# Kernel tuning notes

Measured on AMD Instinct MI355X. Metric: run time of the kernel, lower is better.

## Reference

```python
import jax, jax.numpy as jnp
import numpy as np

B, S, D, H = 4, 1024, 1024, 16
HD = D // H  # head_dim = 64


def setup_inputs() -> dict:
    key = jax.random.key(0)
    ks = jax.random.split(key, 12)
    inp = {
        "query": jax.random.normal(ks[0], (B, S, D), jnp.float32),
        "key": jax.random.normal(ks[1], (B, S, D), jnp.float32),
        "value": jax.random.normal(ks[2], (B, S, D), jnp.float32),
        # padding mask: 0 = masked, 1 = keep; broadcastable to [B,H,Sq,Sk]
        "mask": jax.random.randint(ks[3], (B, 1, 1, S), 0, 2, jnp.int32),
        # Dense params (Glorot-ish scale)
        "Wq": jax.random.normal(ks[4], (D, D), jnp.float32) / np.sqrt(D),
        "bq": jnp.zeros((D,), jnp.float32),
        "Wk": jax.random.normal(ks[5], (D, D), jnp.float32) / np.sqrt(D),
        "bk": jnp.zeros((D,), jnp.float32),
        "Wv": jax.random.normal(ks[6], (D, D), jnp.float32) / np.sqrt(D),
        "bv": jnp.zeros((D,), jnp.float32),
        "Wo": jax.random.normal(ks[7], (D, D), jnp.float32) / np.sqrt(D),
        "bo": jnp.zeros((D,), jnp.float32),
    }
    return inp


def _split_heads(x):
    # [B, S, D] -> [B, H, S, HD]
    b, s, _ = x.shape
    return x.reshape(b, s, H, HD).transpose(0, 2, 1, 3)


def reference(query, key, value, mask, Wq, bq, Wk, bk, Wv, bv, Wo, bo):
    q = _split_heads(query @ Wq + bq)   # [B,H,S,HD]
    k = _split_heads(key @ Wk + bk)
    v = _split_heads(value @ Wv + bv)

    scale = jnp.sqrt(jnp.asarray(HD, q.dtype))
    energy = jnp.einsum("bhqd,bhkd->bhqk", q, k) / scale  # [B,H,S,S]
    energy = jnp.where(mask == 0, jnp.asarray(-1e10, energy.dtype), energy)
    attention = jax.nn.softmax(energy, axis=-1)
    # dropout is identity at inference
    x = jnp.einsum("bhqk,bhkd->bhqd", attention, v)       # [B,H,S,HD]
    x = x.transpose(0, 2, 1, 3).reshape(query.shape[0], -1, H * HD)  # [B,S,D]
    outputs = x @ Wo + bo
    return outputs, attention
```

## Files before the change

kernel.cpp:

```cpp
#include <hip/hip_runtime.h>

typedef short short8  __attribute__((ext_vector_type(8)));
typedef short short4v __attribute__((ext_vector_type(4)));
typedef float float4v __attribute__((ext_vector_type(4)));
typedef int   int4v   __attribute__((ext_vector_type(4)));

__device__ __forceinline__ short f2bf(float f) {
    unsigned u = __builtin_bit_cast(unsigned, f);
    u += 0x7fff + ((u >> 16) & 1);
    return (short)(u >> 16);
}

__global__ __launch_bounds__(256) void transpose4(
    const float* __restrict__ W0, const float* __restrict__ W1,
    const float* __restrict__ W2, const float* __restrict__ W3,
    short* __restrict__ T0, short* __restrict__ T1,
    short* __restrict__ T2, short* __restrict__ T3)
{
    __shared__ short Tl[64 * 72];
    const int tid = threadIdx.x;
    const int mat = blockIdx.x >> 8;
    const int t   = blockIdx.x & 255;
    const int k0 = (t >> 4) * 64, n0 = (t & 15) * 64;
    const float* W = mat == 0 ? W0 : mat == 1 ? W1 : mat == 2 ? W2 : W3;
    short*       T = mat == 0 ? T0 : mat == 1 ? T1 : mat == 2 ? T2 : T3;
    #pragma unroll
    for (int i = 0; i < 4; i++) {
        int c = tid + i * 256;
        int row = c >> 4, c4 = (c & 15) * 4;
        float4v v = *(const float4v*)&W[(size_t)(k0 + row) * 1024 + n0 + c4];
        short4v s = {f2bf(v[0]), f2bf(v[1]), f2bf(v[2]), f2bf(v[3])};
        *(short4v*)&Tl[row * 72 + c4] = s;
    }
    __syncthreads();
    #pragma unroll
    for (int i = 0; i < 2; i++) {
        int c = tid + i * 256;
        int nrow = c >> 3, k8 = (c & 7) * 8;
        short8 v;
        #pragma unroll
        for (int e = 0; e < 8; e++) v[e] = Tl[(k8 + e) * 72 + nrow];
        *(short8*)&T[(size_t)(n0 + nrow) * 1024 + k0 + k8] = v;
    }
}

template<int CMODE, bool A_BF16>
__global__ __launch_bounds__(256) void gemm_bt64(
    const void* __restrict__ Av, const short* __restrict__ Bt,
    const float* __restrict__ bias, void* __restrict__ Cv,
    int M, int N, int K)
{
    __shared__ short As[64 * 72];
    __shared__ short Bs[64 * 72];
    const int tid = threadIdx.x;
    const int m0 = blockIdx.x * 64, n0 = blockIdx.y * 64;
    const int w = tid >> 6, lid = tid & 63, quad = lid >> 4, l15 = lid & 15;
    const int wrow = (w >> 1) * 32, wcol = (w & 1) * 32;

    float4v acc[2][2];
    #pragma unroll
    for (int i = 0; i < 2; i++)
        #pragma unroll
        for (int j = 0; j < 2; j++) acc[i][j] = (float4v){0.f, 0.f, 0.f, 0.f};

    for (int kb = 0; kb < K; kb += 64) {
        if constexpr (A_BF16) {
            const short* A = (const short*)Av;
            #pragma unroll
            for (int i = 0; i < 2; i++) {
                int c = tid + i * 256;
                int row = c >> 3, k8 = (c & 7) * 8;
                *(short8*)&As[row * 72 + k8] =
                    *(const short8*)&A[(size_t)(m0 + row) * K + kb + k8];
            }
        } else {
            const float* A = (const float*)Av;
            #pragma unroll
            for (int i = 0; i < 4; i++) {
                int c = tid + i * 256;
                int row = c >> 4, c4 = (c & 15) * 4;
                float4v v = *(const float4v*)&A[(size_t)(m0 + row) * K + kb + c4];
                short4v s = {f2bf(v[0]), f2bf(v[1]), f2bf(v[2]), f2bf(v[3])};
                *(short4v*)&As[row * 72 + c4] = s;
            }
        }
        #pragma unroll
        for (int i = 0; i < 2; i++) {
            int c = tid + i * 256;
            int row = c >> 3, k8 = (c & 7) * 8;
            *(short8*)&Bs[row * 72 + k8] =
                *(const short8*)&Bt[(size_t)(n0 + row) * K + kb + k8];
        }
        __syncthreads();
        short8 ar0[2], ar1[2], br0[2], br1[2];
        #pragma unroll
        for (int i = 0; i < 2; i++) {
            ar0[i] = *(short8*)&As[(wrow + i * 16 + l15) * 72 + quad * 8];
            ar1[i] = *(short8*)&As[(wrow + i * 16 + l15) * 72 + 32 + quad * 8];
        }
        #pragma unroll
        for (int j = 0; j < 2; j++) {
            br0[j] = *(short8*)&Bs[(wcol + j * 16 + l15) * 72 + quad * 8];
            br1[j] = *(short8*)&Bs[(wcol + j * 16 + l15) * 72 + 32 + quad * 8];
        }
        #pragma unroll
        for (int i = 0; i < 2; i++)
            #pragma unroll
            for (int j = 0; j < 2; j++) {
                acc[i][j] = __builtin_amdgcn_mfma_f32_16x16x32_bf16(
                    ar0[i], br0[j], acc[i][j], 0, 0, 0);
                acc[i][j] = __builtin_amdgcn_mfma_f32_16x16x32_bf16(
                    ar1[i], br1[j], acc[i][j], 0, 0, 0);
            }
        __syncthreads();
    }

    #pragma unroll
    for (int j = 0; j < 2; j++) {
        int n = n0 + wcol + j * 16 + l15;
        float bj = bias[n];
        #pragma unroll
        for (int i = 0; i < 2; i++) {
            if constexpr (CMODE == 2) {
                short* Vt = (short*)Cv;
                int b = m0 >> 10;
                int sbase = (m0 & 1023) + wrow + i * 16 + quad * 4;
                short4v sv;
                #pragma unroll
                for (int r = 0; r < 4; r++) sv[r] = f2bf(acc[i][j][r] + bj);
                *(short4v*)&Vt[(size_t)b * 1048576 + (size_t)n * 1024 + sbase] = sv;
            } else {
                #pragma unroll
                for (int r = 0; r < 4; r++) {
                    int m = m0 + wrow + i * 16 + quad * 4 + r;
                    if constexpr (CMODE == 1)
                        ((float*)Cv)[(size_t)m * N + n] = acc[i][j][r] + bj;
                    else
                        ((short*)Cv)[(size_t)m * N + n] = f2bf(acc[i][j][r] + bj);
                }
            }
        }
    }
}

__global__ __launch_bounds__(256) void attn_kernel(
    const short* __restrict__ Qp, const short* __restrict__ Kp,
    const short* __restrict__ Vt, const int* __restrict__ mask,
    float* __restrict__ attnOut, short* __restrict__ X)
{
    __shared__ short KVl[128 * 72];
    __shared__ short Pl[16 * 136];
    __shared__ int   maskl[1024];
    __shared__ float redmx[4][16];
    __shared__ float redsm[4][16];

    const int tid = threadIdx.x;
    const int w = tid >> 6, lid = tid & 63, quad = lid >> 4, l15 = lid & 15;
    const int bid = blockIdx.x;
    const int qb = bid & 63;
    const int bh = bid >> 6;
    const int b = bh >> 4, h = bh & 15;
    const int q0 = qb * 16;
    const size_t rowbase = (size_t)b * 1048576;

    *(int4v*)&maskl[tid * 4] = *(const int4v*)&mask[b * 1024 + tid * 4];

    short8 aq0 = *(const short8*)
        &Qp[rowbase + (size_t)(q0 + l15) * 1024 + h * 64 + quad * 8];
    short8 aq1 = *(const short8*)
        &Qp[rowbase + (size_t)(q0 + l15) * 1024 + h * 64 + 32 + quad * 8];

    float4v accS[16];
    #pragma unroll
    for (int a = 0; a < 16; a++) accS[a] = (float4v){0.f, 0.f, 0.f, 0.f};

    for (int nk = 0; nk < 8; nk++) {
        #pragma unroll
        for (int i = 0; i < 4; i++) {
            int c = tid + i * 256;
            int row = c >> 3, k8 = (c & 7) * 8;
            *(short8*)&KVl[row * 72 + k8] = *(const short8*)
                &Kp[rowbase + (size_t)(nk * 128 + row) * 1024 + h * 64 + k8];
        }
        __syncthreads();
        #pragma unroll
        for (int jj = 0; jj < 2; jj++) {
            int nloc = w * 32 + jj * 16 + l15;
            short8 b0 = *(short8*)&KVl[nloc * 72 + quad * 8];
            short8 b1 = *(short8*)&KVl[nloc * 72 + 32 + quad * 8];
            int a = nk * 2 + jj;
            accS[a] = __builtin_amdgcn_mfma_f32_16x16x32_bf16(aq0, b0, accS[a], 0, 0, 0);
            accS[a] = __builtin_amdgcn_mfma_f32_16x16x32_bf16(aq1, b1, accS[a], 0, 0, 0);
        }
        __syncthreads();
    }

    float mx[4] = {-3e38f, -3e38f, -3e38f, -3e38f};
    #pragma unroll
    for (int a = 0; a < 16; a++) {
        int col = (a >> 1) * 128 + w * 32 + (a & 1) * 16 + l15;
        bool keep = maskl[col] != 0;
        #pragma unroll
        for (int r = 0; r < 4; r++) {
            float s = accS[a][r] * 0.125f;
            s = keep ? s : -1e10f;
            accS[a][r] = s;
            mx[r] = fmaxf(mx[r], s);
        }
    }
    #pragma unroll
    for (int off = 1; off < 16; off <<= 1)
        #pragma unroll
        for (int r = 0; r < 4; r++) mx[r] = fmaxf(mx[r], __shfl_xor(mx[r], off));
    if (l15 == 0) {
        #pragma unroll
        for (int r = 0; r < 4; r++) redmx[w][quad * 4 + r] = mx[r];
    }
    __syncthreads();
    float mrow[4], sm[4] = {0.f, 0.f, 0.f, 0.f};
    #pragma unroll
    for (int r = 0; r < 4; r++) {
        int qr = quad * 4 + r;
        mrow[r] = fmaxf(fmaxf(redmx[0][qr], redmx[1][qr]),
                        fmaxf(redmx[2][qr], redmx[3][qr]));
    }
    #pragma unroll
    for (int a = 0; a < 16; a++)
        #pragma unroll
        for (int r = 0; r < 4; r++) {
            float e = __expf(accS[a][r] - mrow[r]);
            accS[a][r] = e;
            sm[r] += e;
        }
    #pragma unroll
    for (int off = 1; off < 16; off <<= 1)
        #pragma unroll
        for (int r = 0; r < 4; r++) sm[r] += __shfl_xor(sm[r], off);
    if (l15 == 0) {
        #pragma unroll
        for (int r = 0; r < 4; r++) redsm[w][quad * 4 + r] = sm[r];
    }
    __syncthreads();
    float inv[4];
    #pragma unroll
    for (int r = 0; r < 4; r++) {
        int qr = quad * 4 + r;
        inv[r] = 1.0f / (redsm[0][qr] + redsm[1][qr] + redsm[2][qr] + redsm[3][qr]);
    }

    const size_t abase = ((size_t)bh * 1024 + q0) * 1024;
    float4v accX = (float4v){0.f, 0.f, 0.f, 0.f};
    for (int kt = 0; kt < 8; kt++) {
        #pragma unroll
        for (int i = 0; i < 4; i++) {
            int c = tid + i * 256;
            int row = c >> 4, s8 = (c & 15) * 8;
            *(short8*)&KVl[row * 136 + s8] = *(const short8*)
                &Vt[rowbase + (size_t)(h * 64 + row) * 1024 + kt * 128 + s8];
        }
        #pragma unroll
        for (int jj = 0; jj < 2; jj++) {
            int a = kt * 2 + jj;
            int cl = w * 32 + jj * 16 + l15;
            int col = kt * 128 + cl;
            #pragma unroll
            for (int r = 0; r < 4; r++) {
                float p = accS[a][r] * inv[r];
                attnOut[abase + (size_t)(quad * 4 + r) * 1024 + col] = p;
                Pl[(quad * 4 + r) * 136 + cl] = f2bf(p);
            }
        }
        __syncthreads();
        #pragma unroll
        for (int kk = 0; kk < 4; kk++) {
            short8 ap = *(short8*)&Pl[l15 * 136 + kk * 32 + quad * 8];
            short8 bv = *(short8*)&KVl[(w * 16 + l15) * 136 + kk * 32 + quad * 8];
            accX = __builtin_amdgcn_mfma_f32_16x16x32_bf16(ap, bv, accX, 0, 0, 0);
        }
        __syncthreads();
    }
    #pragma unroll
    for (int r = 0; r < 4; r++)
        X[rowbase + (size_t)(q0 + quad * 4 + r) * 1024 + h * 64 + w * 16 + l15] =
            f2bf(accX[r]);
}

extern "C" void kernel_launch(void* const* d_in, const int* in_sizes, int n_in,
                              void* d_out, int out_size, void* d_ws, size_t ws_size,
                              hipStream_t stream)
{
    const float* q_in = (const float*)d_in[0];
    const float* k_in = (const float*)d_in[1];
    const float* v_in = (const float*)d_in[2];
    const int*   mask = (const int*)d_in[3];
    const float* Wq = (const float*)d_in[4];
    const float* bq = (const float*)d_in[5];
    const float* Wk = (const float*)d_in[6];
    const float* bk = (const float*)d_in[7];
    const float* Wv = (const float*)d_in[8];
    const float* bv = (const float*)d_in[9];
    const float* Wo = (const float*)d_in[10];
    const float* bo = (const float*)d_in[11];

    short* ws = (short*)d_ws;
    const size_t MEL = 4096ull * 1024;
    short* Qp  = ws;
    short* Kp  = ws + MEL;
    short* Vt  = ws + 2 * MEL;
    short* Xp  = ws + 3 * MEL;
    short* WqT = ws + 4 * MEL;
    short* WkT = WqT + 1024 * 1024;
    short* WvT = WkT + 1024 * 1024;
    short* WoT = WvT + 1024 * 1024;

    float* outp  = (float*)d_out;
    float* attnp = outp + MEL;

    transpose4<<<dim3(1024), dim3(256), 0, stream>>>(Wq, Wk, Wv, Wo,
                                                     WqT, WkT, WvT, WoT);
    dim3 gg(64, 16);
    gemm_bt64<0, false><<<gg, 256, 0, stream>>>(q_in, WqT, bq, Qp, 4096, 1024, 1024);
    gemm_bt64<0, false><<<gg, 256, 0, stream>>>(k_in, WkT, bk, Kp, 4096, 1024, 1024);
    gemm_bt64<2, false><<<gg, 256, 0, stream>>>(v_in, WvT, bv, Vt, 4096, 1024, 1024);
    attn_kernel<<<dim3(4096), dim3(256), 0, stream>>>(Qp, Kp, Vt, mask, attnp, Xp);
    gemm_bt64<1, true><<<gg, 256, 0, stream>>>(Xp, WoT, bo, outp, 4096, 1024, 1024);
}
```

Before: 541.1 us.

## Pre-convert inputs to bf16 and use 128x64 GEMM tiles with direct-to-LDS loads

A combined prep kernel transposes the weights and converts the fp32 query/key/value activations to bf16, staging them in the attention-output buffer before that buffer is overwritten. The projection GEMMs become a 128x64 tile kernel that loads A and B with global_load_lds and an XOR-swizzled LDS layout instead of a padded layout with register staging. This aims to cut per-tile fp32 conversion, halve redundant weight reloads and reduce LDS bank conflicts. In exchange it adds an extra pass over the activations and gives each wave more accumulator registers.

```diff
diff --git a/kernel.cpp b/kernel.cpp
--- a/kernel.cpp
+++ b/kernel.cpp
@@ -11,14 +11,36 @@
     return (short)(u >> 16);
 }
 
-__global__ __launch_bounds__(256) void transpose4(
+__device__ __forceinline__ void gl_lds16(const void* g, void* l) {
+    __builtin_amdgcn_global_load_lds(
+        (const __attribute__((address_space(1))) void*)g,
+        (__attribute__((address_space(3))) void*)l, 16, 0, 0);
+}
+
+__global__ __launch_bounds__(256) void prep(
     const float* __restrict__ W0, const float* __restrict__ W1,
     const float* __restrict__ W2, const float* __restrict__ W3,
     short* __restrict__ T0, short* __restrict__ T1,
-    short* __restrict__ T2, short* __restrict__ T3)
+    short* __restrict__ T2, short* __restrict__ T3,
+    const float* __restrict__ qf, const float* __restrict__ kf,
+    const float* __restrict__ vf,
+    short* __restrict__ Qb, short* __restrict__ Kb, short* __restrict__ Vb)
 {
     __shared__ short Tl[64 * 72];
     const int tid = threadIdx.x;
+    if (blockIdx.x >= 1024) {
+        int cid = blockIdx.x - 1024;
+        int arr = cid >> 11;
+        const float* src = arr == 0 ? qf : arr == 1 ? kf : vf;
+        short*       dst = arr == 0 ? Qb : arr == 1 ? Kb : Vb;
+        size_t base = ((size_t)(cid & 2047) * 256 + tid) * 8;
+        float4v v0 = *(const float4v*)&src[base];
+        float4v v1 = *(const float4v*)&src[base + 4];
+        short8 o = {f2bf(v0[0]), f2bf(v0[1]), f2bf(v0[2]), f2bf(v0[3]),
+                    f2bf(v1[0]), f2bf(v1[1]), f2bf(v1[2]), f2bf(v1[3])};
+        *(short8*)&dst[base] = o;
+        return;
+    }
     const int mat = blockIdx.x >> 8;
     const int t   = blockIdx.x & 255;
     const int k0 = (t >> 4) * 64, n0 = (t & 15) * 64;
@@ -44,87 +66,83 @@
     }
 }
 
-template<int CMODE, bool A_BF16>
-__global__ __launch_bounds__(256) void gemm_bt64(
-    const void* __restrict__ Av, const short* __restrict__ Bt,
+template<int CMODE>
+__global__ __launch_bounds__(256) void gemm128(
+    const short* __restrict__ A, const short* __restrict__ Bt,
     const float* __restrict__ bias, void* __restrict__ Cv,
     int M, int N, int K)
 {
-    __shared__ short As[64 * 72];
-    __shared__ short Bs[64 * 72];
+    __shared__ short As[128 * 64];
+    __shared__ short Bs[64 * 64];
     const int tid = threadIdx.x;
-    const int m0 = blockIdx.x * 64, n0 = blockIdx.y * 64;
     const int w = tid >> 6, lid = tid & 63, quad = lid >> 4, l15 = lid & 15;
-    const int wrow = (w >> 1) * 32, wcol = (w & 1) * 32;
-
-    float4v acc[2][2];
-    #pragma unroll
-    for (int i = 0; i < 2; i++)
+    const int wr = w >> 1, wc = w & 1;
+    const int m0 = blockIdx.x * 128, n0 = blockIdx.y * 64;
+    const int lrow = lid >> 3;
+    const int lcb  = lid & 7;
+
+    float4v acc[4][2];
+    #pragma unroll
+    for (int i = 0; i < 4; i++)
         #pragma unroll
         for (int j = 0; j < 2; j++) acc[i][j] = (float4v){0.f, 0.f, 0.f, 0.f};
 
     for (int kb = 0; kb < K; kb += 64) {
-        if constexpr (A_BF16) {
-            const short* A = (const short*)Av;
+        #pragma unroll
+        for (int p = 0; p < 4; p++) {
+            int chunk = p * 4 + w;
+            int row = chunk * 8 + lrow;
+            int cb = lcb ^ (row & 7);
+            gl_lds16(&A[(size_t)(m0 + row) * K + kb + cb * 8], &As[chunk * 512]);
+        }
+        #pragma unroll
+        for (int p = 0; p < 2; p++) {
+            int chunk = p * 4 + w;
+            int row = chunk * 8 + lrow;
+            int cb = lcb ^ (row & 7);
+            gl_lds16(&Bt[(size_t)(n0 + row) * K + kb + cb * 8], &Bs[chunk * 512]);
+        }
+        __syncthreads();
+
+        short8 af[4][2], bfr[2][2];
+        #pragma unroll
+        for (int i = 0; i < 4; i++) {
+            int row = wr * 64 + i * 16 + l15;
+            int sw = row & 7;
             #pragma unroll
-            for (int i = 0; i < 2; i++) {
-                int c = tid + i * 256;
-                int row = c >> 3, k8 = (c & 7) * 8;
-                *(short8*)&As[row * 72 + k8] =
-                    *(const short8*)&A[(size_t)(m0 + row) * K + kb + k8];
-            }
-        } else {
-            const float* A = (const float*)Av;
+            for (int h = 0; h < 2; h++)
+                af[i][h] = *(short8*)&As[row * 64 + ((h * 4 + quad) ^ sw) * 8];
+        }
+        #pragma unroll
+        for (int j = 0; j < 2; j++) {
+            int row = wc * 32 + j * 16 + l15;
+            int sw = row & 7;
             #pragma unroll
-            for (int i = 0; i < 4; i++) {
-                int c = tid + i * 256;
-                int row = c >> 4, c4 = (c & 15) * 4;
-                float4v v = *(const float4v*)&A[(size_t)(m0 + row) * K + kb + c4];
-                short4v s = {f2bf(v[0]), f2bf(v[1]), f2bf(v[2]), f2bf(v[3])};
-                *(short4v*)&As[row * 72 + c4] = s;
-            }
-        }
-        #pragma unroll
-        for (int i = 0; i < 2; i++) {
-            int c = tid + i * 256;
-            int row = c >> 3, k8 = (c & 7) * 8;
-            *(short8*)&Bs[row * 72 + k8] =
-                *(const short8*)&Bt[(size_t)(n0 + row) * K + kb + k8];
-        }
-        __syncthreads();
-        short8 ar0[2], ar1[2], br0[2], br1[2];
-        #pragma unroll
-        for (int i = 0; i < 2; i++) {
-            ar0[i] = *(short8*)&As[(wrow + i * 16 + l15) * 72 + quad * 8];
-            ar1[i] = *(short8*)&As[(wrow + i * 16 + l15) * 72 + 32 + quad * 8];
-        }
-        #pragma unroll
-        for (int j = 0; j < 2; j++) {
-            br0[j] = *(short8*)&Bs[(wcol + j * 16 + l15) * 72 + quad * 8];
-            br1[j] = *(short8*)&Bs[(wcol + j * 16 + l15) * 72 + 32 + quad * 8];
-        }
-        #pragma unroll
-        for (int i = 0; i < 2; i++)
+            for (int h = 0; h < 2; h++)
+                bfr[j][h] = *(short8*)&Bs[row * 64 + ((h * 4 + quad) ^ sw) * 8];
+        }
+        #pragma unroll
+        for (int i = 0; i < 4; i++)
             #pragma unroll
             for (int j = 0; j < 2; j++) {
                 acc[i][j] = __builtin_amdgcn_mfma_f32_16x16x32_bf16(
-                    ar0[i], br0[j], acc[i][j], 0, 0, 0);
+                    af[i][0], bfr[j][0], acc[i][j], 0, 0, 0);
                 acc[i][j] = __builtin_amdgcn_mfma_f32_16x16x32_bf16(
-                    ar1[i], br1[j], acc[i][j], 0, 0, 0);
+                    af[i][1], bfr[j][1], acc[i][j], 0, 0, 0);
             }
         __syncthreads();
     }
 
     #pragma unroll
     for (int j = 0; j < 2; j++) {
-        int n = n0 + wcol + j * 16 + l15;
+        int n = n0 + wc * 32 + j * 16 + l15;
         float bj = bias[n];
         #pragma unroll
-        for (int i = 0; i < 2; i++) {
+        for (int i = 0; i < 4; i++) {
             if constexpr (CMODE == 2) {
                 short* Vt = (short*)Cv;
                 int b = m0 >> 10;
-                int sbase = (m0 & 1023) + wrow + i * 16 + quad * 4;
+                int sbase = (m0 & 1023) + wr * 64 + i * 16 + quad * 4;
                 short4v sv;
                 #pragma unroll
                 for (int r = 0; r < 4; r++) sv[r] = f2bf(acc[i][j][r] + bj);
@@ -132,7 +150,7 @@
             } else {
                 #pragma unroll
                 for (int r = 0; r < 4; r++) {
-                    int m = m0 + wrow + i * 16 + quad * 4 + r;
+                    int m = m0 + wr * 64 + i * 16 + quad * 4 + r;
                     if constexpr (CMODE == 1)
                         ((float*)Cv)[(size_t)m * N + n] = acc[i][j][r] + bj;
                     else
@@ -316,12 +334,17 @@
     float* outp  = (float*)d_out;
     float* attnp = outp + MEL;
 
-    transpose4<<<dim3(1024), dim3(256), 0, stream>>>(Wq, Wk, Wv, Wo,
-                                                     WqT, WkT, WvT, WoT);
-    dim3 gg(64, 16);
-    gemm_bt64<0, false><<<gg, 256, 0, stream>>>(q_in, WqT, bq, Qp, 4096, 1024, 1024);
-    gemm_bt64<0, false><<<gg, 256, 0, stream>>>(k_in, WkT, bk, Kp, 4096, 1024, 1024);
-    gemm_bt64<2, false><<<gg, 256, 0, stream>>>(v_in, WvT, bv, Vt, 4096, 1024, 1024);
+    short* Qb = (short*)attnp;
+    short* Kb = Qb + MEL;
+    short* Vb = Kb + MEL;
+
+    prep<<<dim3(7168), dim3(256), 0, stream>>>(Wq, Wk, Wv, Wo,
+                                               WqT, WkT, WvT, WoT,
+                                               q_in, k_in, v_in, Qb, Kb, Vb);
+    dim3 gg(32, 16);
+    gemm128<0><<<gg, 256, 0, stream>>>(Qb, WqT, bq, Qp, 4096, 1024, 1024);
+    gemm128<0><<<gg, 256, 0, stream>>>(Kb, WkT, bk, Kp, 4096, 1024, 1024);
+    gemm128<2><<<gg, 256, 0, stream>>>(Vb, WvT, bv, Vt, 4096, 1024, 1024);
     attn_kernel<<<dim3(4096), dim3(256), 0, stream>>>(Qp, Kp, Vt, mask, attnp, Xp);
-    gemm_bt64<1, true><<<gg, 256, 0, stream>>>(Xp, WoT, bo, outp, 4096, 1024, 1024);
-}
+    gemm128<1><<<gg, 256, 0, stream>>>(Xp, WoT, bo, outp, 4096, 1024, 1024);
+}
```

New measurement: 542.2 us. About the same (+0.2%).
